# Kernel tuning notes

Hardware: AMD Instinct MI355X
Metric: run time of the kernel (lower is better)

Reference implementation:

```python
import jax, jax.numpy as jnp
import numpy as np


def setup_inputs() -> dict:
    key = jax.random.key(0)
    k1, k2 = jax.random.split(key)
    b, t, f = 64, 2048, 1024
    hidden_decoder = jax.random.normal(k1, (b, f), dtype=jnp.float32)
    hiddens_encoder = jax.random.normal(k2, (b, t, f), dtype=jnp.float32)
    return {"hidden_decoder": hidden_decoder, "hiddens_encoder": hiddens_encoder}


def reference(hidden_decoder, hiddens_encoder):
    # scores[b, t] = <hidden_decoder[b], hiddens_encoder[b, t]>
    # (the original loops over t, computes full bxb matmuls and takes diagonals;
    #  this is the equivalent batched dot product)
    scores = jnp.einsum("bf,btf->bt", hidden_decoder, hiddens_encoder)
    a = jax.nn.softmax(scores, axis=1)  # (b, t)
    # context[b, f] = sum_t a[b, t] * hiddens_encoder[b, t, f]
    context = jnp.einsum("bt,btf->bf", a, hiddens_encoder)
    return context
```

## Files before the change

kernel.cpp:

```cpp
#include <hip/hip_runtime.h>
#include <math.h>


#define BB 64
#define TT 2048
#define FF 1024
#define RR 4
#define NBUF 3

typedef __attribute__((address_space(1))) const void* gas_ptr;
typedef __attribute__((address_space(3))) void* las_ptr;

__device__ __forceinline__ void gld_lds16(const float* g, float* l) {
    __builtin_amdgcn_global_load_lds((gas_ptr)g, (las_ptr)l, 16, 0, 0);
}

__device__ __forceinline__ void stage_row(const float* __restrict__ row,
                                          float* dst, int lane) {
#pragma unroll
    for (int k = 0; k < 4; ++k)
        gld_lds16(row + k * 256 + lane * 4, dst + k * 256);
}

__global__ __launch_bounds__(256) void attn_pass1(
    const float* __restrict__ hd, const float* __restrict__ he,
    float* __restrict__ part_ctx, float* __restrict__ part_m,
    float* __restrict__ part_l, int S, int Tc)
{
    const int bid  = blockIdx.x;
    const int b    = bid / S;
    const int s    = bid - b * S;
    const int t0   = s * Tc;
    const int lane = threadIdx.x & 63;
    const int wave = threadIdx.x >> 6;
    const int nt   = Tc / RR;

    __shared__ __align__(16) float buf[NBUF][RR * FF];
    __shared__ __align__(16) float scores[RR];

    const float* hdb = hd + (size_t)b * FF;
    float4 hdv[4];
#pragma unroll
    for (int k = 0; k < 4; ++k)
        hdv[k] = *(const float4*)(hdb + 4 * lane + 256 * k);

    const float* heb = he + ((size_t)b * TT + t0) * (size_t)FF;

    float m = -INFINITY, l = 0.f;
    float4 ctx = make_float4(0.f, 0.f, 0.f, 0.f);

    stage_row(heb + (size_t)wave * FF, &buf[0][wave * FF], lane);
    stage_row(heb + (size_t)(RR + wave) * FF, &buf[1][wave * FF], lane);

    for (int kt = 0; kt < nt; ++kt) {
        const int cur = kt % NBUF;

        if (kt + 1 < nt) {
            asm volatile("s_waitcnt vmcnt(4)" ::: "memory");
        } else {
            asm volatile("s_waitcnt vmcnt(0)" ::: "memory");
        }
        __builtin_amdgcn_sched_barrier(0);
        __builtin_amdgcn_s_barrier();
        __builtin_amdgcn_sched_barrier(0);

        if (kt + 2 < nt)
            stage_row(heb + ((size_t)(kt + 2) * RR + wave) * FF,
                      &buf[(kt + 2) % NBUF][wave * FF], lane);

        {
            const float* rp = &buf[cur][wave * FF];
            float4 hv[4];
#pragma unroll
            for (int k = 0; k < 4; ++k)
                hv[k] = *(const float4*)(rp + 4 * lane + 256 * k);
            float acc = 0.f;
#pragma unroll
            for (int k = 0; k < 4; ++k)
                acc += hdv[k].x * hv[k].x + hdv[k].y * hv[k].y +
                       hdv[k].z * hv[k].z + hdv[k].w * hv[k].w;
#pragma unroll
            for (int off = 32; off >= 1; off >>= 1)
                acc += __shfl_xor(acc, off, 64);
            if (lane == 0) scores[wave] = acc;
        }

        asm volatile("s_waitcnt lgkmcnt(0)" ::: "memory");
        __builtin_amdgcn_sched_barrier(0);
        __builtin_amdgcn_s_barrier();
        __builtin_amdgcn_sched_barrier(0);

        const float4 sc = *(const float4*)scores;
        float mn = fmaxf(fmaxf(m, fmaxf(sc.x, sc.y)), fmaxf(sc.z, sc.w));
        const float alpha = __expf(m - mn);
        const float w0 = __expf(sc.x - mn), w1 = __expf(sc.y - mn);
        const float w2 = __expf(sc.z - mn), w3 = __expf(sc.w - mn);

        const int f4 = threadIdx.x * 4;
        const float4 r0 = *(const float4*)&buf[cur][0 * FF + f4];
        const float4 r1 = *(const float4*)&buf[cur][1 * FF + f4];
        const float4 r2 = *(const float4*)&buf[cur][2 * FF + f4];
        const float4 r3 = *(const float4*)&buf[cur][3 * FF + f4];
        ctx.x = ctx.x * alpha + w0 * r0.x + w1 * r1.x + w2 * r2.x + w3 * r3.x;
        ctx.y = ctx.y * alpha + w0 * r0.y + w1 * r1.y + w2 * r2.y + w3 * r3.y;
        ctx.z = ctx.z * alpha + w0 * r0.z + w1 * r1.z + w2 * r2.z + w3 * r3.z;
        ctx.w = ctx.w * alpha + w0 * r0.w + w1 * r1.w + w2 * r2.w + w3 * r3.w;
        l = l * alpha + (w0 + w1 + w2 + w3);
        m = mn;
    }

    *(float4*)(part_ctx + (size_t)bid * FF + threadIdx.x * 4) = ctx;
    if (threadIdx.x == 0) { part_m[bid] = m; part_l[bid] = l; }
}

__global__ __launch_bounds__(64) void attn_pass2(
    const float* __restrict__ part_ctx, const float* __restrict__ part_m,
    const float* __restrict__ part_l, float* __restrict__ out, int S)
{
    const int b  = blockIdx.x >> 2;
    const int f4 = ((blockIdx.x & 3) * 64 + threadIdx.x) * 4;

    float M = -INFINITY;
    for (int s = 0; s < S; ++s) M = fmaxf(M, part_m[b * S + s]);
    float L = 0.f;
    for (int s = 0; s < S; ++s)
        L += part_l[b * S + s] * __expf(part_m[b * S + s] - M);

    float4 acc = make_float4(0.f, 0.f, 0.f, 0.f);
    for (int s = 0; s < S; ++s) {
        const float e  = __expf(part_m[b * S + s] - M);
        const float4 c = *(const float4*)(part_ctx + ((size_t)(b * S + s)) * FF + f4);
        acc.x += e * c.x; acc.y += e * c.y; acc.z += e * c.z; acc.w += e * c.w;
    }
    const float inv = 1.f / L;
    *(float4*)(out + (size_t)b * FF + f4) =
        make_float4(acc.x * inv, acc.y * inv, acc.z * inv, acc.w * inv);
}

extern "C" void kernel_launch(void* const* d_in, const int* in_sizes, int n_in,
                              void* d_out, int out_size, void* d_ws, size_t ws_size,
                              hipStream_t stream) {
    const float* hd = (const float*)d_in[0];
    const float* he = (const float*)d_in[1];
    float* out = (float*)d_out;

    int S = 32;
    while (S > 1 && (size_t)BB * S * (FF * sizeof(float) + 2 * sizeof(float)) > ws_size)
        S >>= 1;
    const int Tc = TT / S;

    float* part_ctx = (float*)d_ws;
    float* part_m   = part_ctx + (size_t)BB * S * FF;
    float* part_l   = part_m + (size_t)BB * S;

    attn_pass1<<<BB * S, 256, 0, stream>>>(hd, he, part_ctx, part_m, part_l, S, Tc);
    attn_pass2<<<BB * 4, 64, 0, stream>>>(part_ctx, part_m, part_l, out, S);
}
```

Before: 698.1 us.

## Replace LDS staging with per-wave register double buffering and independent online softmax

Each wave now streams its own rows into registers, prefetching the next row while it computes on the current one. It keeps a private online-softmax state and context vector over the full feature width. This removes the global-to-LDS staging and the two block barriers per iteration. Wave states are merged once at the end through LDS. In exchange it uses more registers per thread and depends on the register prefetch to hide memory latency, whereas the old code overlapped loads through a triple-buffered async pipeline.

```diff
diff --git a/kernel.cpp b/kernel.cpp
--- a/kernel.cpp
+++ b/kernel.cpp
@@ -5,22 +5,6 @@
 #define BB 64
 #define TT 2048
 #define FF 1024
-#define RR 4
-#define NBUF 3
-
-typedef __attribute__((address_space(1))) const void* gas_ptr;
-typedef __attribute__((address_space(3))) void* las_ptr;
-
-__device__ __forceinline__ void gld_lds16(const float* g, float* l) {
-    __builtin_amdgcn_global_load_lds((gas_ptr)g, (las_ptr)l, 16, 0, 0);
-}
-
-__device__ __forceinline__ void stage_row(const float* __restrict__ row,
-                                          float* dst, int lane) {
-#pragma unroll
-    for (int k = 0; k < 4; ++k)
-        gld_lds16(row + k * 256 + lane * 4, dst + k * 256);
-}
 
 __global__ __launch_bounds__(256) void attn_pass1(
     const float* __restrict__ hd, const float* __restrict__ he,
@@ -33,84 +17,92 @@
     const int t0   = s * Tc;
     const int lane = threadIdx.x & 63;
     const int wave = threadIdx.x >> 6;
-    const int nt   = Tc / RR;
+    const int nt   = Tc >> 2;
 
-    __shared__ __align__(16) float buf[NBUF][RR * FF];
-    __shared__ __align__(16) float scores[RR];
+    __shared__ __align__(16) float cbuf[4][FF];
+    __shared__ float wm[4], wl[4];
 
     const float* hdb = hd + (size_t)b * FF;
     float4 hdv[4];
 #pragma unroll
     for (int k = 0; k < 4; ++k)
-        hdv[k] = *(const float4*)(hdb + 4 * lane + 256 * k);
+        hdv[k] = *(const float4*)(hdb + 4 * (lane + 64 * k));
 
     const float* heb = he + ((size_t)b * TT + t0) * (size_t)FF;
 
     float m = -INFINITY, l = 0.f;
-    float4 ctx = make_float4(0.f, 0.f, 0.f, 0.f);
+    float4 ctx[4];
+#pragma unroll
+    for (int k = 0; k < 4; ++k) ctx[k] = make_float4(0.f, 0.f, 0.f, 0.f);
 
-    stage_row(heb + (size_t)wave * FF, &buf[0][wave * FF], lane);
-    stage_row(heb + (size_t)(RR + wave) * FF, &buf[1][wave * FF], lane);
+    float4 cur[4], nxt[4];
+    {
+        const float* r0 = heb + (size_t)wave * FF;
+#pragma unroll
+        for (int k = 0; k < 4; ++k)
+            cur[k] = *(const float4*)(r0 + 4 * (lane + 64 * k));
+    }
 
     for (int kt = 0; kt < nt; ++kt) {
-        const int cur = kt % NBUF;
-
         if (kt + 1 < nt) {
-            asm volatile("s_waitcnt vmcnt(4)" ::: "memory");
-        } else {
-            asm volatile("s_waitcnt vmcnt(0)" ::: "memory");
-        }
-        __builtin_amdgcn_sched_barrier(0);
-        __builtin_amdgcn_s_barrier();
-        __builtin_amdgcn_sched_barrier(0);
-
-        if (kt + 2 < nt)
-            stage_row(heb + ((size_t)(kt + 2) * RR + wave) * FF,
-                      &buf[(kt + 2) % NBUF][wave * FF], lane);
-
-        {
-            const float* rp = &buf[cur][wave * FF];
-            float4 hv[4];
+            const float* rn = heb + ((size_t)(kt + 1) * 4 + wave) * FF;
 #pragma unroll
             for (int k = 0; k < 4; ++k)
-                hv[k] = *(const float4*)(rp + 4 * lane + 256 * k);
-            float acc = 0.f;
-#pragma unroll
-            for (int k = 0; k < 4; ++k)
-                acc += hdv[k].x * hv[k].x + hdv[k].y * hv[k].y +
-                       hdv[k].z * hv[k].z + hdv[k].w * hv[k].w;
-#pragma unroll
-            for (int off = 32; off >= 1; off >>= 1)
-                acc += __shfl_xor(acc, off, 64);
-            if (lane == 0) scores[wave] = acc;
+                nxt[k] = *(const float4*)(rn + 4 * (lane + 64 * k));
         }
 
-        asm volatile("s_waitcnt lgkmcnt(0)" ::: "memory");
-        __builtin_amdgcn_sched_barrier(0);
-        __builtin_amdgcn_s_barrier();
-        __builtin_amdgcn_sched_barrier(0);
+        float d = 0.f;
+#pragma unroll
+        for (int k = 0; k < 4; ++k)
+            d += hdv[k].x * cur[k].x + hdv[k].y * cur[k].y +
+                 hdv[k].z * cur[k].z + hdv[k].w * cur[k].w;
+#pragma unroll
+        for (int off = 32; off >= 1; off >>= 1)
+            d += __shfl_xor(d, off, 64);
 
-        const float4 sc = *(const float4*)scores;
-        float mn = fmaxf(fmaxf(m, fmaxf(sc.x, sc.y)), fmaxf(sc.z, sc.w));
+        const float mn    = fmaxf(m, d);
         const float alpha = __expf(m - mn);
-        const float w0 = __expf(sc.x - mn), w1 = __expf(sc.y - mn);
-        const float w2 = __expf(sc.z - mn), w3 = __expf(sc.w - mn);
+        const float w     = __expf(d - mn);
+#pragma unroll
+        for (int k = 0; k < 4; ++k) {
+            ctx[k].x = ctx[k].x * alpha + w * cur[k].x;
+            ctx[k].y = ctx[k].y * alpha + w * cur[k].y;
+            ctx[k].z = ctx[k].z * alpha + w * cur[k].z;
+            ctx[k].w = ctx[k].w * alpha + w * cur[k].w;
+        }
+        l = l * alpha + w;
+        m = mn;
 
-        const int f4 = threadIdx.x * 4;
-        const float4 r0 = *(const float4*)&buf[cur][0 * FF + f4];
-        const float4 r1 = *(const float4*)&buf[cur][1 * FF + f4];
-        const float4 r2 = *(const float4*)&buf[cur][2 * FF + f4];
-        const float4 r3 = *(const float4*)&buf[cur][3 * FF + f4];
-        ctx.x = ctx.x * alpha + w0 * r0.x + w1 * r1.x + w2 * r2.x + w3 * r3.x;
-        ctx.y = ctx.y * alpha + w0 * r0.y + w1 * r1.y + w2 * r2.y + w3 * r3.y;
-        ctx.z = ctx.z * alpha + w0 * r0.z + w1 * r1.z + w2 * r2.z + w3 * r3.z;
-        ctx.w = ctx.w * alpha + w0 * r0.w + w1 * r1.w + w2 * r2.w + w3 * r3.w;
-        l = l * alpha + (w0 + w1 + w2 + w3);
-        m = mn;
+#pragma unroll
+        for (int k = 0; k < 4; ++k) cur[k] = nxt[k];
     }
 
-    *(float4*)(part_ctx + (size_t)bid * FF + threadIdx.x * 4) = ctx;
-    if (threadIdx.x == 0) { part_m[bid] = m; part_l[bid] = l; }
+    if (lane == 0) { wm[wave] = m; wl[wave] = l; }
+    __syncthreads();
+    const float M = fmaxf(fmaxf(wm[0], wm[1]), fmaxf(wm[2], wm[3]));
+    const float L = wl[0] * __expf(wm[0] - M) + wl[1] * __expf(wm[1] - M) +
+                    wl[2] * __expf(wm[2] - M) + wl[3] * __expf(wm[3] - M);
+    const float e = __expf(m - M);
+#pragma unroll
+    for (int k = 0; k < 4; ++k) {
+        float4 c = ctx[k];
+        c.x *= e; c.y *= e; c.z *= e; c.w *= e;
+        *(float4*)&cbuf[wave][4 * (lane + 64 * k)] = c;
+    }
+    __syncthreads();
+
+    const int j = threadIdx.x;
+    const float4 c0 = *(const float4*)&cbuf[0][4 * j];
+    const float4 c1 = *(const float4*)&cbuf[1][4 * j];
+    const float4 c2 = *(const float4*)&cbuf[2][4 * j];
+    const float4 c3 = *(const float4*)&cbuf[3][4 * j];
+    float4 o;
+    o.x = c0.x + c1.x + c2.x + c3.x;
+    o.y = c0.y + c1.y + c2.y + c3.y;
+    o.z = c0.z + c1.z + c2.z + c3.z;
+    o.w = c0.w + c1.w + c2.w + c3.w;
+    *(float4*)(part_ctx + (size_t)bid * FF + 4 * j) = o;
+    if (threadIdx.x == 0) { part_m[bid] = M; part_l[bid] = L; }
 }
 
 __global__ __launch_bounds__(64) void attn_pass2(
```

New measurement: 695.5 us. Within noise of the previous version (-0.4%).
